# Optimization experiments

Measured on AMD Instinct MI355X. Metric: run time of the kernel, lower is better.

Reference implementation:

```python
import jax, jax.numpy as jnp
import numpy as np

B, S, H = 2, 2048, 1024
E, I = 8, 4096
TOP_K = 2
W_SCALE = 0.02


def setup_inputs() -> dict:
    key = jax.random.key(0)
    k1, k2, k3, k4, k5 = jax.random.split(key, 5)
    return {
        "hidden_states": jax.random.normal(k1, (B, S, H), dtype=jnp.float32),
        "gate_w": jax.random.normal(k2, (H, E), dtype=jnp.float32) * W_SCALE,
        "w1s": jax.random.normal(k3, (E, H, I), dtype=jnp.float32) * W_SCALE,
        "w2s": jax.random.normal(k4, (E, I, H), dtype=jnp.float32) * W_SCALE,
        "w3s": jax.random.normal(k5, (E, H, I), dtype=jnp.float32) * W_SCALE,
    }


def reference(hidden_states, gate_w, w1s, w2s, w3s):
    b, s, h = hidden_states.shape
    x = hidden_states.reshape(-1, h)                      # [T, H]
    # Router: softmax in fp32, top-k, renormalize (matches torch F.softmax(dtype=float) + topk)
    logits = x @ gate_w                                   # [T, E]
    probs = jax.nn.softmax(logits.astype(jnp.float32), axis=-1)
    rw, sel = jax.lax.top_k(probs, TOP_K)                 # [T, K], [T, K]
    rw = rw / jnp.sum(rw, axis=-1, keepdims=True)
    # Per-token combine weight for each expert: [T, E]
    comb = jnp.sum(jax.nn.one_hot(sel, E, dtype=x.dtype) * rw[..., None].astype(x.dtype), axis=1)
    # Expert SwiGLU MLPs; loop over small fixed expert count (same math as grouped GEMM + scatter)
    out = jnp.zeros_like(x)
    for e in range(E):
        inter = jax.nn.silu(x @ w1s[e]) * (x @ w3s[e])    # [T, I]
        out = out + comb[:, e:e + 1] * (inter @ w2s[e])   # [T, H]
    return out.reshape(b, s, h)
```

## Files before the change

kernel.cpp:

```cpp
#include <hip/hip_runtime.h>

#define T_TOK 4096
#define H_DIM 1024
#define I_DIM 4096
#define NE 8
#define INTER_ROWS 9216

typedef _Float16 f16;
typedef _Float16 f16x8 __attribute__((ext_vector_type(8)));
typedef _Float16 f16x4 __attribute__((ext_vector_type(4)));
typedef float f32x4 __attribute__((ext_vector_type(4)));

#define GLOBAL_AS __attribute__((address_space(1)))
#define LDS_AS __attribute__((address_space(3)))

__device__ __forceinline__ void gload_lds16(const void* g, void* l) {
  __builtin_amdgcn_global_load_lds((GLOBAL_AS const unsigned int*)g,
                                   (LDS_AS unsigned int*)l, 16, 0, 0);
}

#define VM0() asm volatile("s_waitcnt vmcnt(0)" ::: "memory")
#define BARF()                          \
  do {                                  \
    asm volatile("" ::: "memory");      \
    __builtin_amdgcn_s_barrier();       \
    asm volatile("" ::: "memory");      \
  } while (0)
#define PRIO1() __builtin_amdgcn_s_setprio(1)
#define PRIO0() __builtin_amdgcn_s_setprio(0)

__global__ void cast_x_kernel(const float* __restrict__ x, f16* __restrict__ xh) {
  int i = blockIdx.x * 256 + threadIdx.x;
  float4 v = reinterpret_cast<const float4*>(x)[i];
  f16x4 o = {(f16)v.x, (f16)v.y, (f16)v.z, (f16)v.w};
  reinterpret_cast<f16x4*>(xh)[i] = o;
}

__global__ __launch_bounds__(256) void transpose_cast_kernel(
    const float* __restrict__ w1s, const float* __restrict__ w3s,
    const float* __restrict__ w2s, f16* __restrict__ w13t, f16* __restrict__ w2t) {
  __shared__ float tile[64][65];
  const int z = blockIdx.z;
  const int tr = threadIdx.x >> 4;
  const int tc = (threadIdx.x & 15) * 4;
  if (z < 16) {
    int e = z & 7;
    const float* in = (z < 8 ? w1s : w3s) + (size_t)e * H_DIM * I_DIM;
    f16* out = w13t + (size_t)e * (2 * H_DIM * I_DIM);
    const int roff = (z < 8) ? 0 : 32;
    const int c0 = blockIdx.x * 64, r0 = blockIdx.y * 64;
#pragma unroll
    for (int i = 0; i < 4; ++i) {
      int r = tr + i * 16;
      float4 v = *reinterpret_cast<const float4*>(&in[(size_t)(r0 + r) * I_DIM + c0 + tc]);
      tile[r][tc] = v.x; tile[r][tc + 1] = v.y; tile[r][tc + 2] = v.z; tile[r][tc + 3] = v.w;
    }
    __syncthreads();
#pragma unroll
    for (int it = 0; it < 2; ++it) {
      int idx = it * 256 + threadIdx.x;
      int oc = idx >> 3;
      int ch = (idx & 7) * 8;
      int cg = c0 + oc;
      int rowo = ((cg >> 5) << 6) + roff + (cg & 31);
      f16x8 h;
#pragma unroll
      for (int j = 0; j < 8; ++j) h[j] = (f16)tile[ch + j][oc];
      *reinterpret_cast<f16x8*>(&out[(size_t)rowo * H_DIM + r0 + ch]) = h;
    }
  } else {
    int e = z - 16;
    const float* in = w2s + (size_t)e * H_DIM * I_DIM;
    f16* out = w2t + (size_t)e * H_DIM * I_DIM;
    const int r0 = blockIdx.x * 64, c0 = blockIdx.y * 64;
#pragma unroll
    for (int i = 0; i < 4; ++i) {
      int r = tr + i * 16;
      float4 v = *reinterpret_cast<const float4*>(&in[(size_t)(r0 + r) * H_DIM + c0 + tc]);
      tile[r][tc] = v.x; tile[r][tc + 1] = v.y; tile[r][tc + 2] = v.z; tile[r][tc + 3] = v.w;
    }
    __syncthreads();
#pragma unroll
    for (int it = 0; it < 2; ++it) {
      int idx = it * 256 + threadIdx.x;
      int oc = idx >> 3;
      int ch = (idx & 7) * 8;
      f16x8 h;
#pragma unroll
      for (int j = 0; j < 8; ++j) h[j] = (f16)tile[ch + j][oc];
      *reinterpret_cast<f16x8*>(&out[(size_t)(c0 + oc) * I_DIM + r0 + ch]) = h;
    }
  }
}

__global__ void router_kernel(const float* __restrict__ x, const float* __restrict__ gw,
                              int* __restrict__ counts, int* __restrict__ lists,
                              float* __restrict__ wgts) {
  const int t = blockIdx.x;
  const int l = threadIdx.x;
  const float* xr = x + (size_t)t * H_DIM;
  float acc[NE];
#pragma unroll
  for (int e = 0; e < NE; ++e) acc[e] = 0.f;
  for (int k = l; k < H_DIM; k += 64) {
    float xv = xr[k];
#pragma unroll
    for (int e = 0; e < NE; ++e) acc[e] += xv * gw[k * NE + e];
  }
#pragma unroll
  for (int e = 0; e < NE; ++e) {
    float v = acc[e];
#pragma unroll
    for (int off = 32; off > 0; off >>= 1) v += __shfl_xor(v, off);
    acc[e] = v;
  }
  if (l == 0) {
    int i1 = 0;
#pragma unroll
    for (int e = 1; e < NE; ++e)
      if (acc[e] > acc[i1]) i1 = e;
    int i2 = (i1 == 0) ? 1 : 0;
#pragma unroll
    for (int e = 0; e < NE; ++e)
      if (e != i1 && acc[e] > acc[i2]) i2 = e;
    float wA = 1.f / (1.f + __expf(acc[i2] - acc[i1]));
    float wB = 1.f - wA;
    int p1 = atomicAdd(&counts[i1], 1);
    lists[i1 * T_TOK + p1] = t;
    wgts[i1 * T_TOK + p1] = wA;
    int p2 = atomicAdd(&counts[i2], 1);
    lists[i2 * T_TOK + p2] = t;
    wgts[i2 * T_TOK + p2] = wB;
  }
}

__global__ void prefix_kernel(const int* __restrict__ counts, int* __restrict__ bases) {
  if (threadIdx.x == 0) {
    int s = 0;
#pragma unroll
    for (int e = 0; e < NE; ++e) {
      bases[e] = s;
      s += (counts[e] + 127) & ~127;
    }
  }
}

#define LDAm(DST, kh, SBASE)                                                      \
  {                                                                               \
    _Pragma("unroll") for (int m_ = 0; m_ < 8; ++m_) {                            \
      int row = wm * 128 + m_ * 16 + lrow;                                        \
      DST[m_] = *reinterpret_cast<const f16x8*>(                                  \
          &SBASE[row * 64 + (((kh)*4 + lk) ^ (row & 7)) * 8]);                    \
    }                                                                             \
  }
#define LDBm(DST, kh, np, SBBASE)                                                 \
  {                                                                               \
    _Pragma("unroll") for (int n_ = 0; n_ < 2; ++n_) {                            \
      int row = wn * 64 + ((np)*2 + n_) * 16 + lrow;                              \
      DST[n_] = *reinterpret_cast<const f16x8*>(                                  \
          &SBBASE[row * 64 + (((kh)*4 + lk) ^ (row & 7)) * 8]);                   \
    }                                                                             \
  }
#define MFm(AF, BF, np)                                                           \
  {                                                                               \
    PRIO1();                                                                      \
    _Pragma("unroll") for (int m_ = 0; m_ < 8; ++m_)                              \
        _Pragma("unroll") for (int n_ = 0; n_ < 2; ++n_)                          \
            acc[m_][(np)*2 + n_] = __builtin_amdgcn_mfma_f32_16x16x32_f16(        \
                AF[m_], BF[n_], acc[m_][(np)*2 + n_], 0, 0, 0);                   \
    PRIO0();                                                                      \
  }

__global__ __launch_bounds__(512, 1) void gemm_a_kernel(
    const f16* __restrict__ xh, const f16* __restrict__ w13t,
    const int* __restrict__ counts, const int* __restrict__ bases,
    const int* __restrict__ lists, f16* __restrict__ inter) {
  const int w = blockIdx.x;
  const int xcd = w & 7, q = w >> 3;
  const int bx = xcd * 4 + (q & 3);
  const int by = q >> 2;
  const int z = blockIdx.z;
  const int cnt = counts[z];
  const int r0 = by * 256;
  if (r0 >= cnt) return;
  const int base = bases[z], pad = (cnt + 127) & ~127;
  const int c0 = bx * 256;
  const int tid = threadIdx.x, lane = tid & 63, wid = tid >> 6;
  const int wm = wid >> 2, wn = wid & 3, lrow = lane & 15, lk = lane >> 4;

  __shared__ __align__(16) f16 lds[2][32768];

  const int* lst = lists + z * T_TOK;
  const f16* w13 = w13t + (size_t)z * (2 * H_DIM * I_DIM);

  const f16* sp[4][2];
  f16* dp[4][2];
#pragma unroll
  for (int j = 0; j < 2; ++j) {
    int cg = (wid * 2 + j) * 64 + lane;
    int rih = cg >> 3;
    int loct = (cg & 7) ^ (rih & 7);
    int t0 = lst[r0 + rih], t1 = lst[r0 + 128 + rih];
    sp[0][j] = xh + (size_t)t0 * H_DIM + loct * 8;
    sp[2][j] = xh + (size_t)t1 * H_DIM + loct * 8;
    sp[1][j] = w13 + (size_t)(c0 + rih) * H_DIM + loct * 8;
    sp[3][j] = w13 + (size_t)(c0 + 128 + rih) * H_DIM + loct * 8;
    dp[0][j] = &lds[0][cg * 8];
    dp[2][j] = &lds[0][8192 + cg * 8];
    dp[1][j] = &lds[0][16384 + cg * 8];
    dp[3][j] = &lds[0][24576 + cg * 8];
  }

#define STG(u, S, K)                                        \
  do {                                                      \
    gload_lds16(sp[u][0] + (K), dp[u][0] + (S)*32768);      \
    gload_lds16(sp[u][1] + (K), dp[u][1] + (S)*32768);      \
  } while (0)

  const f32x4 z4 = {0.f, 0.f, 0.f, 0.f};
  f32x4 acc[8][4];
#pragma unroll
  for (int m = 0; m < 8; ++m)
#pragma unroll
    for (int n = 0; n < 4; ++n) acc[m][n] = z4;

  f16x8 afA[8], afB[8], bfX[2], bfY[2];
  const int NT = H_DIM / 64;

  STG(0, 0, 0); STG(1, 0, 0); STG(2, 0, 0); STG(3, 0, 0);
  VM0(); BARF();
  { const f16* SA = lds[0]; const f16* SB = SA + 16384;
    LDAm(afA, 0, SA); LDBm(bfX, 0, 0, SB); }

  for (int t = 0; t < NT; ++t) {
    const f16* SA = lds[t & 1];
    const f16* SB = SA + 16384;
    const int S = (t + 1) & 1;
    const f16* SA2 = lds[S];
    const f16* SB2 = SA2 + 16384;
    const bool more = (t + 1 < NT);
    const int ks = (t + 1) * 64;
    if (more) { STG(0, S, ks); STG(1, S, ks); }
    LDBm(bfY, 0, 1, SB);
    BARF();
    MFm(afA, bfX, 0);
    if (more) { STG(2, S, ks); STG(3, S, ks); }
    LDAm(afB, 1, SA);
    LDBm(bfX, 1, 0, SB);
    BARF();
    MFm(afA, bfY, 1);
    LDBm(bfY, 1, 1, SB);
    BARF();
    MFm(afB, bfX, 0);
    VM0();
    BARF();
    if (more) { LDAm(afA, 0, SA2); LDBm(bfX, 0, 0, SB2); }
    MFm(afB, bfY, 1);
  }
#undef STG

#pragma unroll
  for (int m = 0; m < 8; ++m)
#pragma unroll
    for (int r = 0; r < 4; ++r) {
      int rowl = wm * 128 + m * 16 + lk * 4 + r;
      if (r0 + rowl < pad) {
        size_t grow = base + r0 + rowl;
#pragma unroll
        for (int n = 0; n < 2; ++n) {
          int col = (c0 >> 1) + wn * 32 + n * 16 + lrow;
          float v1 = acc[m][n][r];
          float v3 = acc[m][n + 2][r];
          float sv = v1 / (1.f + __expf(-v1));
          inter[grow * I_DIM + col] = (f16)(sv * v3);
        }
      }
    }
}

__global__ __launch_bounds__(512, 1) void gemm_b_kernel(
    const f16* __restrict__ inter, const f16* __restrict__ w2t,
    const int* __restrict__ counts, const int* __restrict__ bases,
    const int* __restrict__ lists, const float* __restrict__ wgts,
    float* __restrict__ out) {
  const int w = blockIdx.x;
  const int xcd = w & 7, q = w >> 3;
  const int bx = xcd >> 1;
  const int yid = (xcd & 1) * 16 + q;
  const int rb = yid >> 1, kb = yid & 1;
  const int z = blockIdx.z;
  const int cnt = counts[z];
  const int r0 = rb * 256;
  if (r0 >= cnt) return;
  const int base = bases[z];
  const int c0 = bx * 256;
  const int tid = threadIdx.x, lane = tid & 63, wid = tid >> 6;
  const int wm = wid >> 2, wn = wid & 3, lrow = lane & 15, lk = lane >> 4;

  __shared__ __align__(16) f16 lds[2][32768];

  const int* lst = lists + z * T_TOK;
  const float* wgt = wgts + z * T_TOK;
  const f16* w2 = w2t + (size_t)z * I_DIM * H_DIM;
  const int K0 = kb * 2048;

  const f16* sp[4][2];
  f16* dp[4][2];
#pragma unroll
  for (int j = 0; j < 2; ++j) {
    int cg = (wid * 2 + j) * 64 + lane;
    int rih = cg >> 3;
    int loct = (cg & 7) ^ (rih & 7);
    sp[0][j] = inter + (size_t)(base + r0 + rih) * I_DIM + K0 + loct * 8;
    sp[2][j] = inter + (size_t)(base + r0 + 128 + rih) * I_DIM + K0 + loct * 8;
    sp[1][j] = w2 + (size_t)(c0 + rih) * I_DIM + K0 + loct * 8;
    sp[3][j] = w2 + (size_t)(c0 + 128 + rih) * I_DIM + K0 + loct * 8;
    dp[0][j] = &lds[0][cg * 8];
    dp[2][j] = &lds[0][8192 + cg * 8];
    dp[1][j] = &lds[0][16384 + cg * 8];
    dp[3][j] = &lds[0][24576 + cg * 8];
  }

#define STG(u, S, K)                                        \
  do {                                                      \
    gload_lds16(sp[u][0] + (K), dp[u][0] + (S)*32768);      \
    gload_lds16(sp[u][1] + (K), dp[u][1] + (S)*32768);      \
  } while (0)

  const f32x4 z4 = {0.f, 0.f, 0.f, 0.f};
  f32x4 acc[8][4];
#pragma unroll
  for (int m = 0; m < 8; ++m)
#pragma unroll
    for (int n = 0; n < 4; ++n) acc[m][n] = z4;

  f16x8 afA[8], afB[8], bfX[2], bfY[2];
  const int NT = 2048 / 64;

  STG(0, 0, 0); STG(1, 0, 0); STG(2, 0, 0); STG(3, 0, 0);
  VM0(); BARF();
  { const f16* SA = lds[0]; const f16* SB = SA + 16384;
    LDAm(afA, 0, SA); LDBm(bfX, 0, 0, SB); }

  for (int t = 0; t < NT; ++t) {
    const f16* SA = lds[t & 1];
    const f16* SB = SA + 16384;
    const int S = (t + 1) & 1;
    const f16* SA2 = lds[S];
    const f16* SB2 = SA2 + 16384;
    const bool more = (t + 1 < NT);
    const int ks = (t + 1) * 64;
    if (more) { STG(0, S, ks); STG(1, S, ks); }
    LDBm(bfY, 0, 1, SB);
    BARF();
    MFm(afA, bfX, 0);
    if (more) { STG(2, S, ks); STG(3, S, ks); }
    LDAm(afB, 1, SA);
    LDBm(bfX, 1, 0, SB);
    BARF();
    MFm(afA, bfY, 1);
    LDBm(bfY, 1, 1, SB);
    BARF();
    MFm(afB, bfX, 0);
    VM0();
    BARF();
    if (more) { LDAm(afA, 0, SA2); LDBm(bfX, 0, 0, SB2); }
    MFm(afB, bfY, 1);
  }
#undef STG

#pragma unroll
  for (int m = 0; m < 8; ++m)
#pragma unroll
    for (int r = 0; r < 4; ++r) {
      int ri = r0 + wm * 128 + m * 16 + lk * 4 + r;
      if (ri < cnt) {
        int tok = lst[ri];
        float wg = wgt[ri];
        float* orow = out + (size_t)tok * H_DIM + c0 + wn * 64 + lrow;
#pragma unroll
        for (int n = 0; n < 4; ++n) atomicAdd(&orow[n * 16], wg * acc[m][n][r]);
      }
    }
}

extern "C" void kernel_launch(void* const* d_in, const int* in_sizes, int n_in,
                              void* d_out, int out_size, void* d_ws, size_t ws_size,
                              hipStream_t stream) {
  const float* x = (const float*)d_in[0];
  const float* gw = (const float*)d_in[1];
  const float* w1s = (const float*)d_in[2];
  const float* w2s = (const float*)d_in[3];
  const float* w3s = (const float*)d_in[4];
  float* out = (float*)d_out;

  char* ws = (char*)d_ws;
  f16* xh = (f16*)ws;
  f16* inter = (f16*)(ws + ((size_t)8 << 20));
  f16* w13t = (f16*)(ws + ((size_t)80 << 20));
  f16* w2t = (f16*)(ws + ((size_t)208 << 20));
  char* meta = ws + ((size_t)272 << 20);
  int* counts = (int*)meta;
  int* bases = (int*)(meta + 512);
  int* lists = (int*)(meta + 1024);
  float* wgts = (float*)(meta + 1024 + (size_t)NE * T_TOK * 4);

  hipMemsetAsync(out, 0, (size_t)out_size * sizeof(float), stream);
  hipMemsetAsync(meta, 0, 1024 + (size_t)NE * T_TOK * 8, stream);

  cast_x_kernel<<<dim3((T_TOK * H_DIM) / (4 * 256)), dim3(256), 0, stream>>>(x, xh);
  router_kernel<<<dim3(T_TOK), dim3(64), 0, stream>>>(x, gw, counts, lists, wgts);
  prefix_kernel<<<dim3(1), dim3(64), 0, stream>>>(counts, bases);
  transpose_cast_kernel<<<dim3(64, 16, 24), dim3(256), 0, stream>>>(
      w1s, w3s, w2s, w13t, w2t);
  gemm_a_kernel<<<dim3(512, 1, NE), dim3(512), 0, stream>>>(
      xh, w13t, counts, bases, lists, inter);
  gemm_b_kernel<<<dim3(128, 1, NE), dim3(512), 0, stream>>>(
      inter, w2t, counts, bases, lists, wgts, out);
}
```

Baseline: 611.3 us.

## Shrink gemm_b tiles to 128x128, drop XCD block swizzle, retune transpose stores

The down-projection GEMM moves from 256x256 tiles with 512 threads to 128x128 tiles with 256 threads and two blocks per CU. Each block uses half the LDS and gets more blocks per expert, so small experts leave fewer CUs idle. Both GEMMs drop the XCD-aware block-index remapping in favour of plain 2D grid indexing. The transpose-cast kernel now writes f16x4 per thread instead of f16x8, which risks worse L2 locality across XCDs and less operand reuse per tile.

```diff
diff --git a/kernel.cpp b/kernel.cpp
--- a/kernel.cpp
+++ b/kernel.cpp
@@ -57,16 +57,14 @@
     }
     __syncthreads();
 #pragma unroll
-    for (int it = 0; it < 2; ++it) {
-      int idx = it * 256 + threadIdx.x;
-      int oc = idx >> 3;
-      int ch = (idx & 7) * 8;
+    for (int i = 0; i < 4; ++i) {
+      int oc = tr + i * 16;
       int cg = c0 + oc;
       int rowo = ((cg >> 5) << 6) + roff + (cg & 31);
-      f16x8 h;
-#pragma unroll
-      for (int j = 0; j < 8; ++j) h[j] = (f16)tile[ch + j][oc];
-      *reinterpret_cast<f16x8*>(&out[(size_t)rowo * H_DIM + r0 + ch]) = h;
+      f16x4 h;
+#pragma unroll
+      for (int j = 0; j < 4; ++j) h[j] = (f16)tile[tc + j][oc];
+      *reinterpret_cast<f16x4*>(&out[(size_t)rowo * H_DIM + r0 + tc]) = h;
     }
   } else {
     int e = z - 16;
@@ -81,14 +79,12 @@
     }
     __syncthreads();
 #pragma unroll
-    for (int it = 0; it < 2; ++it) {
-      int idx = it * 256 + threadIdx.x;
-      int oc = idx >> 3;
-      int ch = (idx & 7) * 8;
-      f16x8 h;
-#pragma unroll
-      for (int j = 0; j < 8; ++j) h[j] = (f16)tile[ch + j][oc];
-      *reinterpret_cast<f16x8*>(&out[(size_t)(c0 + oc) * I_DIM + r0 + ch]) = h;
+    for (int i = 0; i < 4; ++i) {
+      int oc = tr + i * 16;
+      f16x4 h;
+#pragma unroll
+      for (int j = 0; j < 4; ++j) h[j] = (f16)tile[tc + j][oc];
+      *reinterpret_cast<f16x4*>(&out[(size_t)(c0 + oc) * I_DIM + r0 + tc]) = h;
     }
   }
 }
@@ -175,16 +171,12 @@
     const f16* __restrict__ xh, const f16* __restrict__ w13t,
     const int* __restrict__ counts, const int* __restrict__ bases,
     const int* __restrict__ lists, f16* __restrict__ inter) {
-  const int w = blockIdx.x;
-  const int xcd = w & 7, q = w >> 3;
-  const int bx = xcd * 4 + (q & 3);
-  const int by = q >> 2;
   const int z = blockIdx.z;
   const int cnt = counts[z];
-  const int r0 = by * 256;
+  const int r0 = blockIdx.y * 256;
   if (r0 >= cnt) return;
   const int base = bases[z], pad = (cnt + 127) & ~127;
-  const int c0 = bx * 256;
+  const int c0 = blockIdx.x * 256;
   const int tid = threadIdx.x, lane = tid & 63, wid = tid >> 6;
   const int wm = wid >> 2, wn = wid & 3, lrow = lane & 15, lk = lane >> 4;
 
@@ -278,102 +270,126 @@
     }
 }
 
-__global__ __launch_bounds__(512, 1) void gemm_b_kernel(
+__global__ __launch_bounds__(256, 2) void gemm_b_kernel(
     const f16* __restrict__ inter, const f16* __restrict__ w2t,
     const int* __restrict__ counts, const int* __restrict__ bases,
     const int* __restrict__ lists, const float* __restrict__ wgts,
     float* __restrict__ out) {
-  const int w = blockIdx.x;
-  const int xcd = w & 7, q = w >> 3;
-  const int bx = xcd >> 1;
-  const int yid = (xcd & 1) * 16 + q;
-  const int rb = yid >> 1, kb = yid & 1;
   const int z = blockIdx.z;
   const int cnt = counts[z];
-  const int r0 = rb * 256;
+  const int rb = blockIdx.y >> 1, kb = blockIdx.y & 1;
+  const int r0 = rb * 128;
   if (r0 >= cnt) return;
   const int base = bases[z];
-  const int c0 = bx * 256;
+  const int c0 = blockIdx.x * 128;
   const int tid = threadIdx.x, lane = tid & 63, wid = tid >> 6;
-  const int wm = wid >> 2, wn = wid & 3, lrow = lane & 15, lk = lane >> 4;
-
-  __shared__ __align__(16) f16 lds[2][32768];
+  const int wm = wid >> 1, wn = wid & 1, lrow = lane & 15, lk = lane >> 4;
+
+  __shared__ __align__(16) f16 lds[2][16384];
 
   const int* lst = lists + z * T_TOK;
   const float* wgt = wgts + z * T_TOK;
   const f16* w2 = w2t + (size_t)z * I_DIM * H_DIM;
   const int K0 = kb * 2048;
 
-  const f16* sp[4][2];
-  f16* dp[4][2];
-#pragma unroll
-  for (int j = 0; j < 2; ++j) {
-    int cg = (wid * 2 + j) * 64 + lane;
-    int rih = cg >> 3;
-    int loct = (cg & 7) ^ (rih & 7);
-    sp[0][j] = inter + (size_t)(base + r0 + rih) * I_DIM + K0 + loct * 8;
-    sp[2][j] = inter + (size_t)(base + r0 + 128 + rih) * I_DIM + K0 + loct * 8;
-    sp[1][j] = w2 + (size_t)(c0 + rih) * I_DIM + K0 + loct * 8;
-    sp[3][j] = w2 + (size_t)(c0 + 128 + rih) * I_DIM + K0 + loct * 8;
-    dp[0][j] = &lds[0][cg * 8];
-    dp[2][j] = &lds[0][8192 + cg * 8];
-    dp[1][j] = &lds[0][16384 + cg * 8];
-    dp[3][j] = &lds[0][24576 + cg * 8];
-  }
-
-#define STG(u, S, K)                                        \
-  do {                                                      \
-    gload_lds16(sp[u][0] + (K), dp[u][0] + (S)*32768);      \
-    gload_lds16(sp[u][1] + (K), dp[u][1] + (S)*32768);      \
+  const f16 *spA[4], *spB[4];
+  f16 *dpA[4], *dpB[4];
+#pragma unroll
+  for (int u = 0; u < 4; ++u) {
+    int cg = u * 256 + tid;
+    int row = cg >> 3;
+    int loct = (cg & 7) ^ (row & 7);
+    spA[u] = inter + (size_t)(base + r0 + row) * I_DIM + K0 + loct * 8;
+    spB[u] = w2 + (size_t)(c0 + row) * I_DIM + K0 + loct * 8;
+    dpA[u] = &lds[0][cg * 8];
+    dpB[u] = &lds[0][8192 + cg * 8];
+  }
+
+#define STGA4(S, K)                                                   \
+  do {                                                                \
+    _Pragma("unroll") for (int u_ = 0; u_ < 4; ++u_)                  \
+        gload_lds16(spA[u_] + (K), dpA[u_] + (S)*16384);              \
   } while (0)
+#define STGB4(S, K)                                                   \
+  do {                                                                \
+    _Pragma("unroll") for (int u_ = 0; u_ < 4; ++u_)                  \
+        gload_lds16(spB[u_] + (K), dpB[u_] + (S)*16384);              \
+  } while (0)
+
+#define LDA2(DST, kh, SBASE)                                                      \
+  {                                                                               \
+    _Pragma("unroll") for (int m_ = 0; m_ < 4; ++m_) {                            \
+      int row = wm * 64 + m_ * 16 + lrow;                                         \
+      DST[m_] = *reinterpret_cast<const f16x8*>(                                  \
+          &SBASE[row * 64 + (((kh)*4 + lk) ^ (row & 7)) * 8]);                    \
+    }                                                                             \
+  }
+#define LDB2(DST, kh, np, SBBASE)                                                 \
+  {                                                                               \
+    _Pragma("unroll") for (int n_ = 0; n_ < 2; ++n_) {                            \
+      int row = wn * 64 + ((np)*2 + n_) * 16 + lrow;                              \
+      DST[n_] = *reinterpret_cast<const f16x8*>(                                  \
+          &SBBASE[row * 64 + (((kh)*4 + lk) ^ (row & 7)) * 8]);                   \
+    }                                                                             \
+  }
+#define MF2(AF, BF, np)                                                           \
+  {                                                                               \
+    PRIO1();                                                                      \
+    _Pragma("unroll") for (int m_ = 0; m_ < 4; ++m_)                              \
+        _Pragma("unroll") for (int n_ = 0; n_ < 2; ++n_)                          \
+            acc[m_][(np)*2 + n_] = __builtin_amdgcn_mfma_f32_16x16x32_f16(        \
+                AF[m_], BF[n_], acc[m_][(np)*2 + n_], 0, 0, 0);                   \
+    PRIO0();                                                                      \
+  }
 
   const f32x4 z4 = {0.f, 0.f, 0.f, 0.f};
-  f32x4 acc[8][4];
-#pragma unroll
-  for (int m = 0; m < 8; ++m)
+  f32x4 acc[4][4];
+#pragma unroll
+  for (int m = 0; m < 4; ++m)
 #pragma unroll
     for (int n = 0; n < 4; ++n) acc[m][n] = z4;
 
-  f16x8 afA[8], afB[8], bfX[2], bfY[2];
+  f16x8 afA[4], afB[4], bfX[2], bfY[2];
   const int NT = 2048 / 64;
 
-  STG(0, 0, 0); STG(1, 0, 0); STG(2, 0, 0); STG(3, 0, 0);
+  STGA4(0, 0); STGB4(0, 0);
   VM0(); BARF();
-  { const f16* SA = lds[0]; const f16* SB = SA + 16384;
-    LDAm(afA, 0, SA); LDBm(bfX, 0, 0, SB); }
+  { const f16* SA = lds[0]; const f16* SB = SA + 8192;
+    LDA2(afA, 0, SA); LDB2(bfX, 0, 0, SB); }
 
   for (int t = 0; t < NT; ++t) {
     const f16* SA = lds[t & 1];
-    const f16* SB = SA + 16384;
+    const f16* SB = SA + 8192;
     const int S = (t + 1) & 1;
     const f16* SA2 = lds[S];
-    const f16* SB2 = SA2 + 16384;
+    const f16* SB2 = SA2 + 8192;
     const bool more = (t + 1 < NT);
     const int ks = (t + 1) * 64;
-    if (more) { STG(0, S, ks); STG(1, S, ks); }
-    LDBm(bfY, 0, 1, SB);
-    BARF();
-    MFm(afA, bfX, 0);
-    if (more) { STG(2, S, ks); STG(3, S, ks); }
-    LDAm(afB, 1, SA);
-    LDBm(bfX, 1, 0, SB);
-    BARF();
-    MFm(afA, bfY, 1);
-    LDBm(bfY, 1, 1, SB);
-    BARF();
-    MFm(afB, bfX, 0);
+    if (more) STGA4(S, ks);
+    LDB2(bfY, 0, 1, SB);
+    BARF();
+    MF2(afA, bfX, 0);
+    if (more) STGB4(S, ks);
+    LDA2(afB, 1, SA);
+    LDB2(bfX, 1, 0, SB);
+    BARF();
+    MF2(afA, bfY, 1);
+    LDB2(bfY, 1, 1, SB);
+    BARF();
+    MF2(afB, bfX, 0);
     VM0();
     BARF();
-    if (more) { LDAm(afA, 0, SA2); LDBm(bfX, 0, 0, SB2); }
-    MFm(afB, bfY, 1);
-  }
-#undef STG
-
-#pragma unroll
-  for (int m = 0; m < 8; ++m)
+    if (more) { LDA2(afA, 0, SA2); LDB2(bfX, 0, 0, SB2); }
+    MF2(afB, bfY, 1);
+  }
+#undef STGA4
+#undef STGB4
+
+#pragma unroll
+  for (int m = 0; m < 4; ++m)
 #pragma unroll
     for (int r = 0; r < 4; ++r) {
-      int ri = r0 + wm * 128 + m * 16 + lk * 4 + r;
+      int ri = r0 + wm * 64 + m * 16 + lk * 4 + r;
       if (ri < cnt) {
         int tok = lst[ri];
         float wg = wgt[ri];
@@ -413,8 +429,8 @@
   prefix_kernel<<<dim3(1), dim3(64), 0, stream>>>(counts, bases);
   transpose_cast_kernel<<<dim3(64, 16, 24), dim3(256), 0, stream>>>(
       w1s, w3s, w2s, w13t, w2t);
-  gemm_a_kernel<<<dim3(512, 1, NE), dim3(512), 0, stream>>>(
+  gemm_a_kernel<<<dim3((2 * I_DIM) / 256, T_TOK / 256, NE), dim3(512), 0, stream>>>(
       xh, w13t, counts, bases, lists, inter);
-  gemm_b_kernel<<<dim3(128, 1, NE), dim3(512), 0, stream>>>(
+  gemm_b_kernel<<<dim3(H_DIM / 128, 2 * (T_TOK / 128), NE), dim3(256), 0, stream>>>(
       inter, w2t, counts, bases, lists, wgts, out);
 }
```

Result: faster. 552.8 us (-9.6%).
